# Kernel tuning notes

Hardware: AMD Instinct MI355X
Metric: run time of the kernel (lower is better)

## Reference

```python
import jax, jax.numpy as jnp
import numpy as np

B, N, L, H = 4, 512, 512, 8
D = 64          # d_model
TAU = 4         # conv dilation
E = 25          # conv kernel size (odd, floor(100/tau))
K = 32          # low_rank_d == top-k
L_OUT = L - TAU * (E - 1)   # 416, n_manifold_embed
EPS = 1e-6


def setup_inputs() -> dict:
    key = jax.random.key(0)
    ks = jax.random.split(key, 7)
    return {
        "x": jax.random.normal(ks[0], (B, N, L, H), jnp.float32),
        "target": jax.random.normal(ks[1], (B, N, L), jnp.float32),
        "conv_w": jax.random.normal(ks[2], (D, H, E), jnp.float32) * 0.05,  # Conv1d weight (out,in,k)
        "proj_w": jax.random.normal(ks[3], (L_OUT,), jnp.float32) * 0.05,   # Linear(L_OUT,1) weight
        "proj_b": jnp.zeros((), jnp.float32),                                # Linear bias
        "W0": jax.random.normal(ks[4], (L, K), jnp.float32) * 0.05,          # low-rank corr proj
        "U0": jax.random.normal(ks[5], (L, K), jnp.float32) * 0.05,
    }


def reference(x, target, conv_w, proj_w, proj_b, W0, U0):
    # --- dilated conv1d manifold embedding: (b n l h) -> ((b n) h l) ---
    xin = jnp.transpose(x.reshape(B * N, L, H), (0, 2, 1))  # (BN, H, L)
    conv = jax.lax.conv_general_dilated(
        xin, conv_w, window_strides=(1,), padding="VALID",
        rhs_dilation=(TAU,), dimension_numbers=("NCH", "OIH", "NCH"))  # (BN, D, L_OUT)
    # conv_out_proj: Linear(L_OUT -> 1) + GELU (exact erf, torch default)
    embed = jax.nn.gelu(conv @ proj_w + proj_b, approximate=False).reshape(B, N, D)

    # --- pearson correlation (computed under no_grad in torch) ---
    v = target - target.mean(axis=-1, keepdims=True)          # (B, N, L)
    vx = v @ W0                                               # (B, N, K)
    vh = v @ U0                                               # (B, N, K)
    num = jnp.einsum("bnk,bmk->bnm", vx, vh)                  # (B, N, N)
    nx = jnp.sqrt(jnp.sum(vx * vx, axis=-1) + EPS)            # (B, N)
    nh = jnp.sqrt(jnp.sum(vh * vh, axis=-1) + EPS)
    pearson = jax.lax.stop_gradient(num / (nx[:, :, None] * nh[:, None, :]))

    # --- top-k sparsification + scatter + softmax normalization ---
    vals, idx = jax.lax.top_k(pearson, K)                     # (B, N, K)
    bi = jnp.arange(B)[:, None, None]
    ni = jnp.arange(N)[None, :, None]
    sparse = jnp.zeros_like(pearson).at[bi, ni, idx].set(vals)  # scatter topk values
    mult = jax.nn.softmax(sparse, axis=-1)                    # F.softmax over full row (zeros included)

    # --- gated attention: sparse correlation graph mixes manifold embeddings ---
    out = jnp.einsum("bnm,bmd->bnd", mult, embed)             # (B, N, D)
    attn = pearson.mean(axis=0)                               # (N, N), returned pearson_cor
    return out, attn
```

## Files before the change

### kernel.cpp

```cpp
#include <hip/hip_runtime.h>
#include <math.h>

#define BB 4
#define NN 512
#define LL 512
#define HH 8
#define DD 64
#define EE 25
#define KK 32
#define LOUT 416
#define EPSF 1e-6f


__global__ void k_transpose_cw(const float* __restrict__ cw, float* __restrict__ Ct) {
    int i = blockIdx.x * 256 + threadIdx.x;
    if (i < DD * HH * EE) {
        int d = i / (HH * EE);
        int he = i % (HH * EE);
        Ct[he * DD + d] = cw[i];
    }
}

__global__ __launch_bounds__(256, 4) void k_embed(
    const float* __restrict__ x, const float* __restrict__ pw,
    const float* __restrict__ pb, const float* __restrict__ Ct,
    float* __restrict__ embedBuf) {
    __shared__ float P[608];
    __shared__ float Sred[4][200];
    __shared__ float Stot[200];
    __shared__ float opart[4][64];
    int tid = threadIdx.x;
    for (int i = tid; i < 608; i += 256) {
        int t = i - 96;
        P[i] = (t >= 0 && t < LOUT) ? pw[t] : 0.f;
    }
    __syncthreads();

    int w = tid >> 6, lane = tid & 63;
    int bn = blockIdx.x;
    const float* xp = x + (size_t)bn * (LL * HH);
    int q = lane >> 3;
    int jb = 16 * w;

    float W[25];
#pragma unroll
    for (int k = 0; k < 25; ++k) W[k] = P[q + 8 * jb + 4 * k];
    float S[25];
#pragma unroll
    for (int e = 0; e < 25; ++e) S[e] = 0.f;

#pragma unroll
    for (int jl = 0; jl < 16; ++jl) {
        int j = jb + jl;
        float v = xp[64 * j + lane];
#pragma unroll
        for (int k = 0; k < 25; ++k)
            S[24 - k] = fmaf(v, W[k], S[24 - k]);
        if (jl < 15) {
#pragma unroll
            for (int k = 0; k < 23; ++k) W[k] = W[k + 2];
            int l = q + 8 * j;
            W[23] = P[l + 100];
            W[24] = P[l + 104];
        }
    }
#pragma unroll
    for (int e = 0; e < 25; ++e) {
        S[e] += __shfl_xor(S[e], 8);
        S[e] += __shfl_xor(S[e], 16);
        S[e] += __shfl_xor(S[e], 32);
    }
    if (lane < 8) {
#pragma unroll
        for (int e = 0; e < 25; ++e) Sred[w][lane * 25 + e] = S[e];
    }
    __syncthreads();
    if (tid < 200)
        Stot[tid] = Sred[0][tid] + Sred[1][tid] + Sred[2][tid] + Sred[3][tid];
    __syncthreads();

    float acc = 0.f;
#pragma unroll 10
    for (int ii = 0; ii < 50; ++ii) {
        int i = 50 * w + ii;
        acc = fmaf(Ct[i * 64 + lane], Stot[i], acc);
    }
    opart[w][lane] = acc;
    __syncthreads();
    if (w == 0) {
        float a = opart[0][lane] + opart[1][lane] + opart[2][lane] + opart[3][lane]
                + pb[0];
        float g = 0.5f * a * (1.f + erff(a * 0.70710678118654752f));
        embedBuf[(size_t)bn * 64 + lane] = g;
    }
}

__global__ __launch_bounds__(256) void k_sumembed(
    const float* __restrict__ embedBuf, float* __restrict__ sumEmbed) {
    int b = blockIdx.x, tid = threadIdx.x;
    int d = tid & 63, c = tid >> 6;
    float s = 0.f;
    for (int r = c; r < 512; r += 4)
        s += embedBuf[((size_t)b * 512 + r) * 64 + d];
    __shared__ float red[4][64];
    red[c][d] = s;
    __syncthreads();
    if (c == 0)
        sumEmbed[b * 64 + d] = red[0][d] + red[1][d] + red[2][d] + red[3][d];
}

__global__ __launch_bounds__(256, 4) void k_corr(
    const float* __restrict__ target, const float* __restrict__ W0,
    const float* __restrict__ U0, float* __restrict__ vxn, float* __restrict__ vhnT) {
    __shared__ float T[2][512];
    __shared__ float mus[2];
    __shared__ float S2[4][2][64];
    int tid = threadIdx.x;
    int w = tid >> 6, lane = tid & 63;
    int r0 = blockIdx.x * 2;

    const float4* tp = (const float4*)(target + (size_t)r0 * 512);
    ((float4*)&T[0][0])[tid] = tp[tid];
    __syncthreads();

    if (w < 2) {
        float s = 0.f;
#pragma unroll
        for (int c = 0; c < 8; ++c) s += T[w][lane + 64 * c];
#pragma unroll
        for (int off = 1; off < 64; off <<= 1) s += __shfl_xor(s, off);
        if (lane == 0) mus[w] = s * (1.f / 512.f);
    }
    __syncthreads();
#pragma unroll
    for (int c = 0; c < 4; ++c) {
        int i = tid + c * 256;
        T[i >> 9][i & 511] -= mus[i >> 9];
    }
    __syncthreads();

    const float* base = (lane < 32) ? W0 : U0;
    int k = lane & 31;
    float acc0 = 0.f, acc1 = 0.f;
    int l0 = w * 128;
#pragma unroll 4
    for (int li = 0; li < 128; ++li) {
        int l = l0 + li;
        float wv = base[l * 32 + k];
        acc0 = fmaf(wv, T[0][l], acc0);
        acc1 = fmaf(wv, T[1][l], acc1);
    }
    S2[w][0][lane] = acc0;
    S2[w][1][lane] = acc1;
    __syncthreads();

    if (w < 2) {
        int r = w;
        float tot = S2[0][r][lane] + S2[1][r][lane] + S2[2][r][lane] + S2[3][r][lane];
        float sq = tot * tot;
#pragma unroll
        for (int off = 1; off < 32; off <<= 1) sq += __shfl_xor(sq, off);
        float o = tot / sqrtf(sq + EPSF);
        int row = r0 + r, b = row >> 9, n = row & 511;
        if (lane < 32) vxn[(size_t)row * 32 + lane] = o;
        else           vhnT[(size_t)b * (32 * 512) + (lane - 32) * 512 + n] = o;
    }
}

__device__ __forceinline__ unsigned long long mkkey(float v, int m) {
    unsigned u = __float_as_uint(v);
    u = (u & 0x80000000u) ? ~u : (u | 0x80000000u);
    return ((unsigned long long)u << 9) | (unsigned)(511 - m);
}

__global__ __launch_bounds__(256, 4) void k_attn(
    const float* __restrict__ vxn, const float* __restrict__ vhnT,
    const float* __restrict__ embedBuf, const float* __restrict__ sumEmbed,
    float* __restrict__ outO, float* __restrict__ outA) {
    __shared__ float candVal[128];
    __shared__ int   candIdx[128];
    __shared__ float sSelVal[32];
    __shared__ int   sSelIdx[32];
    __shared__ float opart[4][64];
    __shared__ float esum[4];
    __shared__ float sM[1];
    int tid = threadIdx.x, w = tid >> 6, lane = tid & 63;
    int bid = blockIdx.x;
    int b = bid >> 9, n = bid & 511;

    const float* vxp = vxn + ((size_t)(b * 512 + n)) * 32;
    float xk[32];
#pragma unroll
    for (int k = 0; k < 32; ++k) xk[k] = vxp[k];

    int m0 = w * 128 + lane;
    const float* vt = vhnT + (size_t)b * (32 * 512);
    float a0 = 0.f, a1 = 0.f;
#pragma unroll
    for (int k = 0; k < 32; ++k) {
        float v0 = vt[k * 512 + m0];
        float v1 = vt[k * 512 + m0 + 64];
        a0 = fmaf(xk[k], v0, a0);
        a1 = fmaf(xk[k], v1, a1);
    }
    atomicAdd(&outA[(size_t)n * 512 + m0], 0.25f * a0);
    atomicAdd(&outA[(size_t)n * 512 + m0 + 64], 0.25f * a1);

    unsigned long long k0 = mkkey(a0, m0), k1 = mkkey(a1, m0 + 64);
    unsigned long long prefix = 0ull;
    for (int bit = 40; bit >= 0; --bit) {
        unsigned long long cand = prefix | (1ull << bit);
        int cnt = __popcll(__ballot(k0 >= cand)) + __popcll(__ballot(k1 >= cand));
        if (cnt >= KK) prefix = cand;
    }
    bool s0 = (k0 >= prefix), s1 = (k1 >= prefix);
    unsigned long long b0 = __ballot(s0), b1 = __ballot(s1);
    unsigned long long lm = lane ? (~0ull >> (64 - lane)) : 0ull;
    int basec = w * 32;
    if (s0) { int sl = basec + __popcll(b0 & lm); candVal[sl] = a0; candIdx[sl] = m0; }
    if (s1) { int sl = basec + __popcll(b0) + __popcll(b1 & lm);
              candVal[sl] = a1; candIdx[sl] = m0 + 64; }
    __syncthreads();

    if (w == 0) {
        float v0 = candVal[lane],  v1 = candVal[64 + lane];
        int   i0 = candIdx[lane],  i1 = candIdx[64 + lane];
        unsigned long long c0 = mkkey(v0, i0), c1 = mkkey(v1, i1);
        unsigned long long pfx = 0ull;
        for (int bit = 40; bit >= 0; --bit) {
            unsigned long long cand = pfx | (1ull << bit);
            int cnt = __popcll(__ballot(c0 >= cand)) + __popcll(__ballot(c1 >= cand));
            if (cnt >= KK) pfx = cand;
        }
        bool t0 = (c0 >= pfx), t1 = (c1 >= pfx);
        unsigned long long d0 = __ballot(t0), d1 = __ballot(t1);
        if (t0) { int sl = __popcll(d0 & lm); sSelVal[sl] = v0; sSelIdx[sl] = i0; }
        if (t1) { int sl = __popcll(d0) + __popcll(d1 & lm);
                  sSelVal[sl] = v1; sSelIdx[sl] = i1; }
        float mx = fmaxf(v0, v1);
#pragma unroll
        for (int off = 1; off < 64; off <<= 1) mx = fmaxf(mx, __shfl_xor(mx, off));
        if (lane == 0) sM[0] = fmaxf(mx, 0.f);
    }
    __syncthreads();

    float M = sM[0];
    float enM = __expf(-M);
    float oacc = 0.f, es = 0.f;
    const float* eb = embedBuf + (size_t)b * 512 * 64;
#pragma unroll
    for (int i = 0; i < 8; ++i) {
        int idx = sSelIdx[w * 8 + i];
        float wv = __expf(sSelVal[w * 8 + i] - M);
        es += wv;
        oacc = fmaf(wv - enM, eb[(size_t)idx * 64 + lane], oacc);
    }
    opart[w][lane] = oacc;
    if (lane == 0) esum[w] = es;
    __syncthreads();
    if (w == 0) {
        float o = opart[0][lane] + opart[1][lane] + opart[2][lane] + opart[3][lane];
        float E = esum[0] + esum[1] + esum[2] + esum[3] + (float)(NN - KK) * enM;
        o = fmaf(enM, sumEmbed[b * 64 + lane], o);
        outO[((size_t)(b * 512 + n)) * 64 + lane] = o / E;
    }
}

extern "C" void kernel_launch(void* const* d_in, const int* in_sizes, int n_in,
                              void* d_out, int out_size, void* d_ws, size_t ws_size,
                              hipStream_t stream) {
    const float* x      = (const float*)d_in[0];
    const float* target = (const float*)d_in[1];
    const float* cw     = (const float*)d_in[2];
    const float* pw     = (const float*)d_in[3];
    const float* pb     = (const float*)d_in[4];
    const float* W0     = (const float*)d_in[5];
    const float* U0     = (const float*)d_in[6];

    float* out  = (float*)d_out;
    float* attn = out + 4 * 512 * 64;

    float* ws       = (float*)d_ws;
    float* embedBuf = ws;
    float* sumEmbed = ws + 131072;
    float* vxn      = ws + 131328;
    float* vhnT     = ws + 196864;
    float* Ct       = ws + 262400;

    hipMemsetAsync(attn, 0, 512 * 512 * sizeof(float), stream);
    k_transpose_cw<<<50, 256, 0, stream>>>(cw, Ct);
    k_embed<<<2048, 256, 0, stream>>>(x, pw, pb, Ct, embedBuf);
    k_sumembed<<<4, 256, 0, stream>>>(embedBuf, sumEmbed);
    k_corr<<<1024, 256, 0, stream>>>(target, W0, U0, vxn, vhnT);
    k_attn<<<2048, 256, 0, stream>>>(vxn, vhnT, embedBuf, sumEmbed, out, attn);
}
```

Before: 161.8 us.

## Fuse embed and corr kernels, replace atomic attn mean with partial buffer

Merges the conv-embedding and Pearson-projection kernels into one launch that picks its role from blockIdx, so the two independent stages overlap on the GPU. The per-batch pearson rows are written to a workspace buffer and reduced by a new k_mean kernel, which replaces the memset plus float atomicAdds on the attention output. Also widens k_sumembed to 1024 threads, raises k_attn's occupancy hint, and broadcasts the query vector through readfirstlane. The cost is an extra 4 MB write and read of partial pearson values plus one more launch.

```diff
diff --git a/kernel.cpp b/kernel.cpp
--- a/kernel.cpp
+++ b/kernel.cpp
@@ -21,149 +21,156 @@
     }
 }
 
-__global__ __launch_bounds__(256, 4) void k_embed(
+__global__ __launch_bounds__(256, 4) void k_fused(
     const float* __restrict__ x, const float* __restrict__ pw,
     const float* __restrict__ pb, const float* __restrict__ Ct,
-    float* __restrict__ embedBuf) {
+    float* __restrict__ embedBuf,
+    const float* __restrict__ target, const float* __restrict__ W0,
+    const float* __restrict__ U0, float* __restrict__ vxn,
+    float* __restrict__ vhnT) {
     __shared__ float P[608];
     __shared__ float Sred[4][200];
     __shared__ float Stot[200];
     __shared__ float opart[4][64];
+    __shared__ float T[2][512];
+    __shared__ float mus[2];
+    __shared__ float S2[4][2][64];
+
     int tid = threadIdx.x;
-    for (int i = tid; i < 608; i += 256) {
-        int t = i - 96;
-        P[i] = (t >= 0 && t < LOUT) ? pw[t] : 0.f;
-    }
-    __syncthreads();
-
     int w = tid >> 6, lane = tid & 63;
-    int bn = blockIdx.x;
-    const float* xp = x + (size_t)bn * (LL * HH);
-    int q = lane >> 3;
-    int jb = 16 * w;
-
-    float W[25];
-#pragma unroll
-    for (int k = 0; k < 25; ++k) W[k] = P[q + 8 * jb + 4 * k];
-    float S[25];
-#pragma unroll
-    for (int e = 0; e < 25; ++e) S[e] = 0.f;
-
-#pragma unroll
-    for (int jl = 0; jl < 16; ++jl) {
-        int j = jb + jl;
-        float v = xp[64 * j + lane];
-#pragma unroll
-        for (int k = 0; k < 25; ++k)
-            S[24 - k] = fmaf(v, W[k], S[24 - k]);
-        if (jl < 15) {
-#pragma unroll
-            for (int k = 0; k < 23; ++k) W[k] = W[k + 2];
-            int l = q + 8 * j;
-            W[23] = P[l + 100];
-            W[24] = P[l + 104];
-        }
-    }
-#pragma unroll
-    for (int e = 0; e < 25; ++e) {
-        S[e] += __shfl_xor(S[e], 8);
-        S[e] += __shfl_xor(S[e], 16);
-        S[e] += __shfl_xor(S[e], 32);
-    }
-    if (lane < 8) {
-#pragma unroll
-        for (int e = 0; e < 25; ++e) Sred[w][lane * 25 + e] = S[e];
-    }
-    __syncthreads();
-    if (tid < 200)
-        Stot[tid] = Sred[0][tid] + Sred[1][tid] + Sred[2][tid] + Sred[3][tid];
-    __syncthreads();
-
-    float acc = 0.f;
+    int bid = blockIdx.x;
+    int sel = bid % 3;
+
+    if (sel != 2) {
+        int bn = (bid / 3) * 2 + sel;
+        for (int i = tid; i < 608; i += 256) {
+            int t = i - 96;
+            P[i] = (t >= 0 && t < LOUT) ? pw[t] : 0.f;
+        }
+        __syncthreads();
+
+        const float* xp = x + (size_t)bn * (LL * HH);
+        int q = lane >> 3;
+        int jb = 16 * w;
+
+        float W[25];
+#pragma unroll
+        for (int k = 0; k < 25; ++k) W[k] = P[q + 8 * jb + 4 * k];
+        float S[25];
+#pragma unroll
+        for (int e = 0; e < 25; ++e) S[e] = 0.f;
+
+#pragma unroll
+        for (int jl = 0; jl < 16; ++jl) {
+            int j = jb + jl;
+            float v = xp[64 * j + lane];
+#pragma unroll
+            for (int k = 0; k < 25; ++k)
+                S[24 - k] = fmaf(v, W[k], S[24 - k]);
+            if (jl < 15) {
+#pragma unroll
+                for (int k = 0; k < 23; ++k) W[k] = W[k + 2];
+                int l = q + 8 * j;
+                W[23] = P[l + 100];
+                W[24] = P[l + 104];
+            }
+        }
+#pragma unroll
+        for (int e = 0; e < 25; ++e) {
+            S[e] += __shfl_xor(S[e], 8);
+            S[e] += __shfl_xor(S[e], 16);
+            S[e] += __shfl_xor(S[e], 32);
+        }
+        if (lane < 8) {
+#pragma unroll
+            for (int e = 0; e < 25; ++e) Sred[w][lane * 25 + e] = S[e];
+        }
+        __syncthreads();
+        if (tid < 200)
+            Stot[tid] = Sred[0][tid] + Sred[1][tid] + Sred[2][tid] + Sred[3][tid];
+        __syncthreads();
+
+        float acc = 0.f;
 #pragma unroll 10
-    for (int ii = 0; ii < 50; ++ii) {
-        int i = 50 * w + ii;
-        acc = fmaf(Ct[i * 64 + lane], Stot[i], acc);
-    }
-    opart[w][lane] = acc;
-    __syncthreads();
-    if (w == 0) {
-        float a = opart[0][lane] + opart[1][lane] + opart[2][lane] + opart[3][lane]
-                + pb[0];
-        float g = 0.5f * a * (1.f + erff(a * 0.70710678118654752f));
-        embedBuf[(size_t)bn * 64 + lane] = g;
-    }
-}
-
-__global__ __launch_bounds__(256) void k_sumembed(
+        for (int ii = 0; ii < 50; ++ii) {
+            int i = 50 * w + ii;
+            acc = fmaf(Ct[i * 64 + lane], Stot[i], acc);
+        }
+        opart[w][lane] = acc;
+        __syncthreads();
+        if (w == 0) {
+            float a = opart[0][lane] + opart[1][lane] + opart[2][lane]
+                    + opart[3][lane] + pb[0];
+            float g = 0.5f * a * (1.f + erff(a * 0.70710678118654752f));
+            embedBuf[(size_t)bn * 64 + lane] = g;
+        }
+    } else {
+        int r0 = (bid / 3) * 2;
+        const float4* tp = (const float4*)(target + (size_t)r0 * 512);
+        ((float4*)&T[0][0])[tid] = tp[tid];
+        __syncthreads();
+
+        if (w < 2) {
+            float s = 0.f;
+#pragma unroll
+            for (int c = 0; c < 8; ++c) s += T[w][lane + 64 * c];
+#pragma unroll
+            for (int off = 1; off < 64; off <<= 1) s += __shfl_xor(s, off);
+            if (lane == 0) mus[w] = s * (1.f / 512.f);
+        }
+        __syncthreads();
+#pragma unroll
+        for (int c = 0; c < 4; ++c) {
+            int i = tid + c * 256;
+            T[i >> 9][i & 511] -= mus[i >> 9];
+        }
+        __syncthreads();
+
+        const float* base = (lane < 32) ? W0 : U0;
+        int k = lane & 31;
+        float acc0 = 0.f, acc1 = 0.f;
+        int l0 = w * 128;
+#pragma unroll 4
+        for (int li = 0; li < 128; ++li) {
+            int l = l0 + li;
+            float wv = base[l * 32 + k];
+            acc0 = fmaf(wv, T[0][l], acc0);
+            acc1 = fmaf(wv, T[1][l], acc1);
+        }
+        S2[w][0][lane] = acc0;
+        S2[w][1][lane] = acc1;
+        __syncthreads();
+
+        if (w < 2) {
+            int r = w;
+            float tot = S2[0][r][lane] + S2[1][r][lane] + S2[2][r][lane]
+                      + S2[3][r][lane];
+            float sq = tot * tot;
+#pragma unroll
+            for (int off = 1; off < 32; off <<= 1) sq += __shfl_xor(sq, off);
+            float o = tot / sqrtf(sq + EPSF);
+            int row = r0 + r, b = row >> 9, n = row & 511;
+            if (lane < 32) vxn[(size_t)row * 32 + lane] = o;
+            else           vhnT[(size_t)b * (32 * 512) + (lane - 32) * 512 + n] = o;
+        }
+    }
+}
+
+__global__ __launch_bounds__(1024) void k_sumembed(
     const float* __restrict__ embedBuf, float* __restrict__ sumEmbed) {
     int b = blockIdx.x, tid = threadIdx.x;
     int d = tid & 63, c = tid >> 6;
     float s = 0.f;
-    for (int r = c; r < 512; r += 4)
+    for (int r = c; r < 512; r += 16)
         s += embedBuf[((size_t)b * 512 + r) * 64 + d];
-    __shared__ float red[4][64];
+    __shared__ float red[16][64];
     red[c][d] = s;
     __syncthreads();
-    if (c == 0)
-        sumEmbed[b * 64 + d] = red[0][d] + red[1][d] + red[2][d] + red[3][d];
-}
-
-__global__ __launch_bounds__(256, 4) void k_corr(
-    const float* __restrict__ target, const float* __restrict__ W0,
-    const float* __restrict__ U0, float* __restrict__ vxn, float* __restrict__ vhnT) {
-    __shared__ float T[2][512];
-    __shared__ float mus[2];
-    __shared__ float S2[4][2][64];
-    int tid = threadIdx.x;
-    int w = tid >> 6, lane = tid & 63;
-    int r0 = blockIdx.x * 2;
-
-    const float4* tp = (const float4*)(target + (size_t)r0 * 512);
-    ((float4*)&T[0][0])[tid] = tp[tid];
-    __syncthreads();
-
-    if (w < 2) {
-        float s = 0.f;
-#pragma unroll
-        for (int c = 0; c < 8; ++c) s += T[w][lane + 64 * c];
-#pragma unroll
-        for (int off = 1; off < 64; off <<= 1) s += __shfl_xor(s, off);
-        if (lane == 0) mus[w] = s * (1.f / 512.f);
-    }
-    __syncthreads();
-#pragma unroll
-    for (int c = 0; c < 4; ++c) {
-        int i = tid + c * 256;
-        T[i >> 9][i & 511] -= mus[i >> 9];
-    }
-    __syncthreads();
-
-    const float* base = (lane < 32) ? W0 : U0;
-    int k = lane & 31;
-    float acc0 = 0.f, acc1 = 0.f;
-    int l0 = w * 128;
-#pragma unroll 4
-    for (int li = 0; li < 128; ++li) {
-        int l = l0 + li;
-        float wv = base[l * 32 + k];
-        acc0 = fmaf(wv, T[0][l], acc0);
-        acc1 = fmaf(wv, T[1][l], acc1);
-    }
-    S2[w][0][lane] = acc0;
-    S2[w][1][lane] = acc1;
-    __syncthreads();
-
-    if (w < 2) {
-        int r = w;
-        float tot = S2[0][r][lane] + S2[1][r][lane] + S2[2][r][lane] + S2[3][r][lane];
-        float sq = tot * tot;
-#pragma unroll
-        for (int off = 1; off < 32; off <<= 1) sq += __shfl_xor(sq, off);
-        float o = tot / sqrtf(sq + EPSF);
-        int row = r0 + r, b = row >> 9, n = row & 511;
-        if (lane < 32) vxn[(size_t)row * 32 + lane] = o;
-        else           vhnT[(size_t)b * (32 * 512) + (lane - 32) * 512 + n] = o;
+    if (c == 0) {
+        float t = 0.f;
+#pragma unroll
+        for (int j = 0; j < 16; ++j) t += red[j][d];
+        sumEmbed[b * 64 + d] = t;
     }
 }
 
@@ -173,10 +180,10 @@
     return ((unsigned long long)u << 9) | (unsigned)(511 - m);
 }
 
-__global__ __launch_bounds__(256, 4) void k_attn(
+__global__ __launch_bounds__(256, 8) void k_attn(
     const float* __restrict__ vxn, const float* __restrict__ vhnT,
     const float* __restrict__ embedBuf, const float* __restrict__ sumEmbed,
-    float* __restrict__ outO, float* __restrict__ outA) {
+    float* __restrict__ outO, float* __restrict__ pbuf) {
     __shared__ float candVal[128];
     __shared__ int   candIdx[128];
     __shared__ float sSelVal[32];
@@ -191,7 +198,9 @@
     const float* vxp = vxn + ((size_t)(b * 512 + n)) * 32;
     float xk[32];
 #pragma unroll
-    for (int k = 0; k < 32; ++k) xk[k] = vxp[k];
+    for (int k = 0; k < 32; ++k)
+        xk[k] = __uint_as_float(__builtin_amdgcn_readfirstlane(
+                    __float_as_uint(vxp[k])));
 
     int m0 = w * 128 + lane;
     const float* vt = vhnT + (size_t)b * (32 * 512);
@@ -203,8 +212,9 @@
         a0 = fmaf(xk[k], v0, a0);
         a1 = fmaf(xk[k], v1, a1);
     }
-    atomicAdd(&outA[(size_t)n * 512 + m0], 0.25f * a0);
-    atomicAdd(&outA[(size_t)n * 512 + m0 + 64], 0.25f * a1);
+    float* pr = pbuf + ((size_t)(b * 512 + n)) * 512;
+    pr[m0] = a0;
+    pr[m0 + 64] = a1;
 
     unsigned long long k0 = mkkey(a0, m0), k1 = mkkey(a1, m0 + 64);
     unsigned long long prefix = 0ull;
@@ -264,6 +274,13 @@
         o = fmaf(enM, sumEmbed[b * 64 + lane], o);
         outO[((size_t)(b * 512 + n)) * 64 + lane] = o / E;
     }
+}
+
+__global__ __launch_bounds__(256) void k_mean(
+    const float* __restrict__ pbuf, float* __restrict__ outA) {
+    int i = blockIdx.x * 256 + threadIdx.x;
+    float s = pbuf[i] + pbuf[262144 + i] + pbuf[524288 + i] + pbuf[786432 + i];
+    outA[i] = 0.25f * s;
 }
 
 extern "C" void kernel_launch(void* const* d_in, const int* in_sizes, int n_in,
@@ -286,11 +303,12 @@
     float* vxn      = ws + 131328;
     float* vhnT     = ws + 196864;
     float* Ct       = ws + 262400;
-
-    hipMemsetAsync(attn, 0, 512 * 512 * sizeof(float), stream);
+    float* pbuf     = ws + 275200;
+
     k_transpose_cw<<<50, 256, 0, stream>>>(cw, Ct);
-    k_embed<<<2048, 256, 0, stream>>>(x, pw, pb, Ct, embedBuf);
-    k_sumembed<<<4, 256, 0, stream>>>(embedBuf, sumEmbed);
-    k_corr<<<1024, 256, 0, stream>>>(target, W0, U0, vxn, vhnT);
-    k_attn<<<2048, 256, 0, stream>>>(vxn, vhnT, embedBuf, sumEmbed, out, attn);
-}
+    k_fused<<<3072, 256, 0, stream>>>(x, pw, pb, Ct, embedBuf,
+                                      target, W0, U0, vxn, vhnT);
+    k_sumembed<<<4, 1024, 0, stream>>>(embedBuf, sumEmbed);
+    k_attn<<<2048, 256, 0, stream>>>(vxn, vhnT, embedBuf, sumEmbed, out, pbuf);
+    k_mean<<<1024, 256, 0, stream>>>(pbuf, attn);
+}
```

Result: faster. 135.4 us (-16.3%).
